# Optimization experiments

Measured on AMD Instinct MI355X. Metric: run time of the kernel, lower is better.

Reference implementation:

```python
import jax, jax.numpy as jnp
import numpy as np

NUM_LAYER = 5
EMB = 300
N_NODES = 100000
N_EDGES = 200000
NUM_GRAPHS = 5000
NUM_ATOM_TYPE = 120
NUM_CHIRALITY = 3
NUM_BOND_TYPE = 6
NUM_BOND_DIR = 3
BN_EPS = 1e-5


def _xavier(key, shape):
    fan_in, fan_out = shape[-2], shape[-1]
    a = jnp.sqrt(6.0 / (fan_in + fan_out))
    return jax.random.uniform(key, shape, jnp.float32, -a, a)


def setup_inputs() -> dict:
    key = jax.random.key(0)
    ks = jax.random.split(key, 12)
    x = jax.random.randint(ks[0], (N_NODES, 2), 0, 3)
    edge_index = jax.random.randint(ks[1], (2, N_EDGES), 0, N_NODES)
    edge_attr = jax.random.randint(ks[2], (N_EDGES, 2), 0, 3)
    batch = jnp.sort(jax.random.randint(ks[3], (N_NODES,), 0, NUM_GRAPHS))
    # parameters (layer-stacked for the NUM_LAYER GIN convs)
    x_emb1 = _xavier(ks[4], (NUM_ATOM_TYPE, EMB))
    x_emb2 = _xavier(ks[5], (NUM_CHIRALITY, EMB))
    edge_e1 = _xavier(ks[6], (NUM_LAYER, NUM_BOND_TYPE, EMB))
    edge_e2 = _xavier(ks[7], (NUM_LAYER, NUM_BOND_DIR, EMB))
    W1 = _xavier(ks[8], (NUM_LAYER, EMB, 2 * EMB))
    b1 = jnp.zeros((NUM_LAYER, 2 * EMB), jnp.float32)
    W2 = _xavier(ks[9], (NUM_LAYER, 2 * EMB, EMB))
    b2 = jnp.zeros((NUM_LAYER, EMB), jnp.float32)
    gamma = jnp.ones((NUM_LAYER, EMB), jnp.float32)
    beta = jnp.zeros((NUM_LAYER, EMB), jnp.float32)
    return dict(x=x, edge_index=edge_index, edge_attr=edge_attr, batch=batch,
                x_emb1=x_emb1, x_emb2=x_emb2, edge_e1=edge_e1, edge_e2=edge_e2,
                W1=W1, b1=b1, W2=W2, b2=b2, gamma=gamma, beta=beta)


def _forward(x, edge_index, edge_attr, batch,
             x_emb1, x_emb2, edge_e1, edge_e2, W1, b1, W2, b2, gamma, beta):
    N = x.shape[0]
    # add self loops (GINConv uses fill_value=0 for self-loop edge_attr)
    loop = jnp.arange(N)
    src = jnp.concatenate([edge_index[0], loop])  # [E+N]
    dst = jnp.concatenate([edge_index[1], loop])
    ea = jnp.concatenate([edge_attr, jnp.zeros((N, 2), edge_attr.dtype)], axis=0)
    h = x_emb1[x[:, 0]] + x_emb2[x[:, 1]]  # [N, EMB]
    for l in range(NUM_LAYER):
        eemb = edge_e1[l][ea[:, 0]] + edge_e2[l][ea[:, 1]]  # [E+N, EMB]
        msg = h[src] + eemb
        agg = jax.ops.segment_sum(msg, dst, num_segments=N)  # scatter-add
        # GIN MLP: Linear(EMB,2EMB) -> ReLU -> Linear(2EMB,EMB)
        h2 = jax.nn.relu(agg @ W1[l] + b1[l]) @ W2[l] + b2[l]
        # BatchNorm1d (training-mode batch statistics, biased var)
        mu = jnp.mean(h2, axis=0)
        var = jnp.mean(jnp.square(h2 - mu), axis=0)
        hn = (h2 - mu) * jax.lax.rsqrt(var + BN_EPS) * gamma[l] + beta[l]
        h = hn if l == NUM_LAYER - 1 else jax.nn.relu(hn)  # drop_ratio=0
    # JK='last'; global mean pool per graph
    sums = jax.ops.segment_sum(h, batch, num_segments=NUM_GRAPHS)
    counts = jax.ops.segment_sum(jnp.ones((N,), h.dtype), batch, num_segments=NUM_GRAPHS)
    return sums / jnp.maximum(counts, 1.0)[:, None]


def reference(x, edge_index, edge_attr, batch,
              x_emb1, x_emb2, edge_e1, edge_e2, W1, b1, W2, b2, gamma, beta):
    return _forward(x, edge_index, edge_attr, batch,
                    x_emb1, x_emb2, edge_e1, edge_e2, W1, b1, W2, b2, gamma, beta)
```

## Files before the change

kernel.cpp:

```cpp
#include <hip/hip_runtime.h>

typedef unsigned short u16;
typedef unsigned int u32;
typedef __attribute__((ext_vector_type(8))) short short8;
typedef __attribute__((ext_vector_type(4))) float float4v;
typedef _Float16 half8v __attribute__((ext_vector_type(8)));

static constexpr int   kN    = 100000;
static constexpr int   kE    = 200000;
static constexpr int   kEMB  = 300;
static constexpr int   kSA   = 304;
static constexpr int   kKW1  = 320;
static constexpr int   kNH   = 600;
static constexpr int   kNHP  = 608;
static constexpr int   kG    = 5000;
static constexpr int   kL    = 5;
static constexpr float kEPS  = 1e-5f;

static constexpr int   kB1BUF = 5120;
static constexpr int   kB2OFF = 10240;
static constexpr int   kB2BUF = 9728;
static constexpr int   kSMEMU = 29696;

__device__ inline float bf2f(u16 u) {
    union { u32 u32v; float f; } v; v.u32v = ((u32)u) << 16; return v.f;
}
__device__ inline u16 f2bf(float f) {
    union { float f; u32 u; } v; v.f = f;
    u32 r = v.u + 0x7fff + ((v.u >> 16) & 1);
    return (u16)(r >> 16);
}
__device__ inline short h16s(float f) {
    union { _Float16 h; short s; } u; u.h = (_Float16)f; return u.s;
}
__device__ inline short8 load8(const u16* p) {
    return *reinterpret_cast<const short8*>(p);
}
__device__ inline half8v as_h8(short8 s) {
    union { short8 s; half8v h; } u; u.s = s; return u.h;
}
__device__ inline float4v zed4() { float4v z = {0.f, 0.f, 0.f, 0.f}; return z; }
__device__ inline float gload(const void* p, long long i, int isf32) {
    if (isf32) return ((const float*)p)[i];
    return bf2f(((const u16*)p)[i]);
}
__device__ inline float pread(const void* p, size_t i, int f32p) {
    if (f32p) return ((const float*)p)[i];
    return bf2f(((const u16*)p)[i]);
}
__device__ inline void pwrite(void* p, size_t i, float v, int f32p) {
    if (f32p) ((float*)p)[i] = v;
    else      ((u16*)p)[i] = f2bf(v);
}
__device__ inline void gl_lds16(const void* g, void* l) {
    __builtin_amdgcn_global_load_lds(
        (__attribute__((address_space(1))) void*)g,
        (__attribute__((address_space(3))) void*)l, 16, 0, 0);
}

__global__ void detect_kernel(const u16* __restrict__ w1raw, int* flag) {
    if (threadIdx.x == 0 && blockIdx.x == 0) {
        int cnt = 0;
        for (int i = 0; i < 256; ++i) {
            int e = (w1raw[i] >> 7) & 0xFF;
            if (e >= 96 && e <= 126) ++cnt;
        }
        *flag = (cnt >= 200) ? 0 : 1;
    }
}

__global__ void cvt_kernel(const void* __restrict__ src, float* __restrict__ dst,
                           int n, const int* __restrict__ flag) {
    int i = blockIdx.x * blockDim.x + threadIdx.x;
    if (i >= n) return;
    int isf = *flag;
    dst[i] = isf ? ((const float*)src)[i] : bf2f(((const u16*)src)[i]);
}

__global__ void w1t_kernel(const void* __restrict__ W1, u16* __restrict__ W1T,
                           const int* __restrict__ flag, int f32p) {
    int idx = blockIdx.x * blockDim.x + threadIdx.x;
    const int per_layer = kNHP * kKW1;
    if (idx >= kL * per_layer) return;
    int isf = *flag;
    int l = idx / per_layer; int rem = idx - l * per_layer;
    int n = rem / kKW1; int k = rem - n * kKW1;
    u16 v = 0;
    if (n < kNH && k < kEMB) {
        float f = gload(W1, (long long)l * kEMB * kNH + (long long)k * kNH + n, isf);
        v = f32p ? (u16)h16s(f) : f2bf(f);
    }
    W1T[idx] = v;
}
__global__ void w2t_kernel(const void* __restrict__ W2, u16* __restrict__ W2T,
                           const int* __restrict__ flag, int f32p) {
    int idx = blockIdx.x * blockDim.x + threadIdx.x;
    const int per_layer = 19 * 304 * 32;
    if (idx >= kL * per_layer) return;
    int isf = *flag;
    int l = idx / per_layer; int rem = idx - l * per_layer;
    int p = rem / (304 * 32); int r2 = rem - p * (304 * 32);
    int n = r2 >> 5; int kk = r2 & 31;
    int q = kk >> 3, j3 = kk & 7;
    int klocal = (j3 < 4) ? (q * 4 + j3) : (16 + q * 4 + (j3 - 4));
    int k = p * 32 + klocal;
    u16 v = 0;
    if (n < kEMB && k < kNH) {
        float f = gload(W2, (long long)l * kNH * kEMB + (long long)k * kEMB + n, isf);
        v = f32p ? (u16)h16s(f) : f2bf(f);
    }
    W2T[idx] = v;
}

__global__ void embed_kernel(const int* __restrict__ x,
                             const float* __restrict__ emb1,
                             const float* __restrict__ emb2,
                             void* __restrict__ h, int f32p) {
    int idx = blockIdx.x * blockDim.x + threadIdx.x;
    if (idx >= kN * kSA) return;
    int n = idx / kSA; int c = idx - n * kSA;
    float v = 0.f;
    if (c < kEMB) v = emb1[x[2 * n] * kEMB + c] + emb2[x[2 * n + 1] * kEMB + c];
    pwrite(h, idx, v, f32p);
}

__global__ void zero_int_kernel(int* p, int n) {
    int i = blockIdx.x * blockDim.x + threadIdx.x;
    if (i < n) p[i] = 0;
}
__global__ void count_kernel(const int* __restrict__ dst, int* row_ptr) {
    int e = blockIdx.x * blockDim.x + threadIdx.x;
    if (e < kE) atomicAdd(&row_ptr[1 + dst[e]], 1);
}
__global__ __launch_bounds__(1024) void scan1_kernel(int* a, int* bsum, int n) {
    __shared__ int s[1024];
    int t = threadIdx.x;
    int i = blockIdx.x * 1024 + t;
    s[t] = (i < n) ? a[i] : 0;
    __syncthreads();
    for (int off = 1; off < 1024; off <<= 1) {
        int v = (t >= off) ? s[t - off] : 0;
        __syncthreads();
        s[t] += v;
        __syncthreads();
    }
    if (i < n) a[i] = s[t];
    if (t == 1023) bsum[blockIdx.x] = s[t];
}
__global__ __launch_bounds__(128) void scan2_kernel(const int* bsum, int* ebsum, int nb) {
    __shared__ int s[128];
    int t = threadIdx.x;
    int orig = (t < nb) ? bsum[t] : 0;
    s[t] = orig;
    __syncthreads();
    for (int off = 1; off < 128; off <<= 1) {
        int v = (t >= off) ? s[t - off] : 0;
        __syncthreads();
        s[t] += v;
        __syncthreads();
    }
    if (t < nb) ebsum[t] = s[t] - orig;
}
__global__ void scan3_kernel(int* a, const int* ebsum, int* row_ptr0, int n) {
    int i = blockIdx.x * blockDim.x + threadIdx.x;
    if (i >= n) return;
    a[i] += ebsum[i >> 10];
    if (i == 0) *row_ptr0 = 0;
}
__global__ void scatter_kernel(const int* __restrict__ src, const int* __restrict__ dst,
                               const int* __restrict__ ea,
                               const int* __restrict__ row_ptr, int* cursor,
                               int* __restrict__ epack) {
    int e = blockIdx.x * blockDim.x + threadIdx.x;
    if (e >= kE) return;
    int d = dst[e];
    int pos = row_ptr[d] + atomicAdd(&cursor[d], 1);
    epack[pos] = src[e] | (ea[2 * e] << 20) | (ea[2 * e + 1] << 24);
}

__global__ __launch_bounds__(256) void aggregate_kernel(
        const void* __restrict__ h, const int* __restrict__ row_ptr,
        const int* __restrict__ epack,
        const float* __restrict__ e1,
        const float* __restrict__ e2,
        const float* __restrict__ stats_prev,
        const float* __restrict__ gam,
        const float* __restrict__ bet,
        float* __restrict__ stats_next,
        void* __restrict__ agg, int mode, int f32p) {
    if (blockIdx.x == 0) {
        for (int i = threadIdx.x; i < 2 * kEMB; i += 256) stats_next[i] = 0.f;
    }
    int wave = threadIdx.x >> 6;
    int lane = threadIdx.x & 63;
    int base = (blockIdx.x * 4 + wave) * 4;

    float sc[5], sh[5];
#pragma unroll
    for (int j = 0; j < 5; ++j) {
        int c = j * 64 + lane;
        sc[j] = 1.f; sh[j] = 0.f;
        if (mode && c < kEMB) {
            const float invM = 1.0f / kN;
            float mu = stats_prev[c] * invM;
            float var = stats_prev[kEMB + c] * invM - mu * mu;
            if (var < 0.f) var = 0.f;
            float rs = rsqrtf(var + kEPS);
            sc[j] = rs * gam[c];
            sh[j] = bet[c] - mu * sc[j];
        }
    }

    int s[4], e[4];
    float acc[4][5];
#pragma unroll
    for (int t = 0; t < 4; ++t) {
        int node = base + t;
        if (node < kN) { s[t] = row_ptr[node]; e[t] = row_ptr[node + 1]; }
        else           { s[t] = 0; e[t] = 0; }
#pragma unroll
        for (int j = 0; j < 5; ++j) {
            int c = j * 64 + lane;
            acc[t][j] = 0.f;
            if (node < kN && c < kEMB) {
                float hv = pread(h, (size_t)node * kSA + c, f32p) * sc[j] + sh[j];
                if (mode && hv < 0.f) hv = 0.f;
                acc[t][j] = hv + e1[c] + e2[c];
            }
        }
    }

    int maxd = 0;
#pragma unroll
    for (int t = 0; t < 4; ++t) {
        int d = e[t] - s[t];
        if (d > maxd) maxd = d;
    }

    for (int i = 0; i < maxd; ++i) {
        int p[4], act[4];
#pragma unroll
        for (int t = 0; t < 4; ++t) {
            act[t] = (s[t] + i < e[t]);
            p[t] = act[t] ? epack[s[t] + i] : 0;
        }
        float hv[4][5];
#pragma unroll
        for (int t = 0; t < 4; ++t) {
            if (act[t]) {
                int srcn = p[t] & 0xFFFFF;
#pragma unroll
                for (int j = 0; j < 5; ++j) {
                    int c = j * 64 + lane;
                    hv[t][j] = (c < kEMB) ? pread(h, (size_t)srcn * kSA + c, f32p) : 0.f;
                }
            }
        }
#pragma unroll
        for (int t = 0; t < 4; ++t) {
            if (act[t]) {
                int a0 = (p[t] >> 20) & 15;
                int a1 = (p[t] >> 24) & 15;
#pragma unroll
                for (int j = 0; j < 5; ++j) {
                    int c = j * 64 + lane;
                    if (c < kEMB) {
                        float w = hv[t][j] * sc[j] + sh[j];
                        if (mode && w < 0.f) w = 0.f;
                        acc[t][j] += w + e1[a0 * kEMB + c] + e2[a1 * kEMB + c];
                    }
                }
            }
        }
    }

#pragma unroll
    for (int t = 0; t < 4; ++t) {
        int node = base + t;
        if (node < kN) {
#pragma unroll
            for (int j = 0; j < 5; ++j) {
                int c = j * 64 + lane;
                if (c < kSA)
                    pwrite(agg, (size_t)node * kSA + c, (c < kEMB) ? acc[t][j] : 0.f, f32p);
            }
        }
    }
}

template <int F32P>
__global__ __launch_bounds__(256, 2) void mlp_kernel(
        const void* A, void* D,
        const u16* __restrict__ W1Tl,
        const float* __restrict__ bias1,
        const u16* __restrict__ W2Tl,
        const float* __restrict__ bias2,
        float* __restrict__ stats) {
    __shared__ __align__(16) u16 SMEM[kSMEMU];
    int tid = threadIdx.x;
    int wave = tid >> 6, lane = tid & 63;
    int r16 = lane & 15, quad = lane >> 4;
    const int NT = kN / 16;
    int mt_raw = blockIdx.x * 4 + wave;
    int mt = (mt_raw < NT) ? mt_raw : (NT - 1);
    int valid = (mt_raw < NT);

#pragma unroll
    for (int i = 0; i < 8; ++i) {
        int c = wave + 4 * i;
        if (c < 10) {
            gl_lds16(W1Tl + (size_t)r16 * kKW1 + c * 32 + quad * 8,
                     SMEM + c * 512);
        } else if (c < 29) {
            int nt2 = c - 10;
            gl_lds16(W2Tl + ((size_t)nt2 * 16 + r16) * 32 + quad * 8,
                     SMEM + kB2OFF + nt2 * 512);
        }
    }

    short8 ahi[10];
    short8 zed = {0, 0, 0, 0, 0, 0, 0, 0};
    if (F32P) {
        const float* Arow = (const float*)A + (size_t)(mt * 16 + r16) * kSA + quad * 8;
#pragma unroll
        for (int kc = 0; kc < 10; ++kc) {
            short8 hh = zed;
            if (kc < 9 || quad < 2) {
                const float* pp = Arow + kc * 32;
#pragma unroll
                for (int j = 0; j < 8; ++j) hh[j] = h16s(pp[j]);
            }
            ahi[kc] = hh;
        }
    } else {
        const u16* Arow = (const u16*)A + (size_t)(mt * 16 + r16) * kSA + quad * 8;
#pragma unroll
        for (int kc = 0; kc < 9; ++kc) ahi[kc] = load8(Arow + kc * 32);
        ahi[9] = (quad < 2) ? load8(Arow + 9 * 32) : zed;
    }

    float4v acc2[19];
#pragma unroll
    for (int i = 0; i < 19; ++i) acc2[i] = zed4();

    short8 a2 = zed;
    short8 a2l = zed;

    for (int p = 0; p < 19; ++p) {
        __syncthreads();
        {
            int p1 = p + 1;
            u16* b1d = SMEM + kB1BUF;
            u16* b2d = SMEM + kB2OFF + (p1 & 1) * kB2BUF;
#pragma unroll
            for (int i = 0; i < 5; ++i) {
                int c = wave + 4 * i;
                if (c < 10) {
                    gl_lds16(W1Tl + (size_t)((2 * p + 1) * 16 + r16) * kKW1
                                 + c * 32 + quad * 8,
                             b1d + c * 512);
                } else if (c < 20 && p1 < 19) {
                    int nt2 = c - 10;
                    gl_lds16(W2Tl + ((size_t)p1 * 304 + nt2 * 16 + r16) * 32 + quad * 8,
                             b2d + nt2 * 512);
                }
            }
        }
        {
            const u16* B1 = SMEM;
            float4v aa = zed4(), ab = zed4();
#pragma unroll
            for (int kc = 0; kc < 10; kc += 2) {
                short8 w0 = load8(B1 + kc * 512 + lane * 8);
                short8 w1 = load8(B1 + (kc + 1) * 512 + lane * 8);
                if (F32P) {
                    aa = __builtin_amdgcn_mfma_f32_16x16x32_f16(as_h8(w0), as_h8(ahi[kc]), aa, 0, 0, 0);
                    ab = __builtin_amdgcn_mfma_f32_16x16x32_f16(as_h8(w1), as_h8(ahi[kc + 1]), ab, 0, 0, 0);
                } else {
                    aa = __builtin_amdgcn_mfma_f32_16x16x32_bf16(w0, ahi[kc], aa, 0, 0, 0);
                    ab = __builtin_amdgcn_mfma_f32_16x16x32_bf16(w1, ahi[kc + 1], ab, 0, 0, 0);
                }
            }
            float4v bv = *(const float4v*)(bias1 + (2 * p) * 16 + quad * 4);
#pragma unroll
            for (int r = 0; r < 4; ++r) {
                int n1 = (2 * p) * 16 + quad * 4 + r;
                float v = (n1 < kNH) ? (aa[r] + ab[r] + bv[r]) : 0.f;
                if (v < 0.f) v = 0.f;
                if (F32P) {
                    a2[r] = h16s(v);
                } else {
                    u16 hb = f2bf(v);
                    a2[r] = (short)hb;
                    a2l[r] = (short)f2bf(v - bf2f(hb));
                }
            }
        }
        __syncthreads();
        {
            int p1 = p + 1;
            u16* b1d = SMEM;
            u16* b2d = SMEM + kB2OFF + (p1 & 1) * kB2BUF;
#pragma unroll
            for (int i = 0; i < 5; ++i) {
                int c = wave + 4 * i;
                if (c < 10) {
                    if (2 * p + 2 < 38)
                        gl_lds16(W1Tl + (size_t)((2 * p + 2) * 16 + r16) * kKW1
                                     + c * 32 + quad * 8,
                                 b1d + c * 512);
                } else {
                    int nt2 = c;
                    if (nt2 < 19 && p1 < 19)
                        gl_lds16(W2Tl + ((size_t)p1 * 304 + nt2 * 16 + r16) * 32 + quad * 8,
                                 b2d + nt2 * 512);
                }
            }
        }
        {
            const u16* B1 = SMEM + kB1BUF;
            float4v aa = zed4(), ab = zed4();
#pragma unroll
            for (int kc = 0; kc < 10; kc += 2) {
                short8 w0 = load8(B1 + kc * 512 + lane * 8);
                short8 w1 = load8(B1 + (kc + 1) * 512 + lane * 8);
                if (F32P) {
                    aa = __builtin_amdgcn_mfma_f32_16x16x32_f16(as_h8(w0), as_h8(ahi[kc]), aa, 0, 0, 0);
                    ab = __builtin_amdgcn_mfma_f32_16x16x32_f16(as_h8(w1), as_h8(ahi[kc + 1]), ab, 0, 0, 0);
                } else {
                    aa = __builtin_amdgcn_mfma_f32_16x16x32_bf16(w0, ahi[kc], aa, 0, 0, 0);
                    ab = __builtin_amdgcn_mfma_f32_16x16x32_bf16(w1, ahi[kc + 1], ab, 0, 0, 0);
                }
            }
            float4v bv = *(const float4v*)(bias1 + (2 * p + 1) * 16 + quad * 4);
#pragma unroll
            for (int r = 0; r < 4; ++r) {
                int n1 = (2 * p + 1) * 16 + quad * 4 + r;
                float v = (n1 < kNH) ? (aa[r] + ab[r] + bv[r]) : 0.f;
                if (v < 0.f) v = 0.f;
                if (F32P) {
                    a2[4 + r] = h16s(v);
                } else {
                    u16 hb = f2bf(v);
                    a2[4 + r] = (short)hb;
                    a2l[4 + r] = (short)f2bf(v - bf2f(hb));
                }
            }
        }
        {
            const u16* B2 = SMEM + kB2OFF + (p & 1) * kB2BUF;
#pragma unroll
            for (int nt2 = 0; nt2 < 19; ++nt2) {
                short8 b = load8(B2 + nt2 * 512 + lane * 8);
                if (F32P) {
                    acc2[nt2] = __builtin_amdgcn_mfma_f32_16x16x32_f16(as_h8(a2), as_h8(b), acc2[nt2], 0, 0, 0);
                } else {
                    acc2[nt2] = __builtin_amdgcn_mfma_f32_16x16x32_bf16(a2, b, acc2[nt2], 0, 0, 0);
                    acc2[nt2] = __builtin_amdgcn_mfma_f32_16x16x32_bf16(a2l, b, acc2[nt2], 0, 0, 0);
                }
            }
        }
    }

    __syncthreads();
    float* RB = (float*)SMEM;
#pragma unroll
    for (int nt2 = 0; nt2 < 19; ++nt2) {
        int n = nt2 * 16 + r16;
        float s4 = 0.f, q4 = 0.f;
        if (valid && n < kEMB) {
            float bv = bias2[n];
#pragma unroll
            for (int r = 0; r < 4; ++r) {
                float v = acc2[nt2][r] + bv;
                int m = mt * 16 + quad * 4 + r;
                pwrite(D, (size_t)m * kSA + n, v, F32P);
                s4 += v; q4 += v * v;
            }
        }
        s4 += __shfl_down(s4, 32); q4 += __shfl_down(q4, 32);
        s4 += __shfl_down(s4, 16); q4 += __shfl_down(q4, 16);
        if (quad == 0) {
            RB[wave * 304 + nt2 * 16 + r16] = s4;
            RB[1216 + wave * 304 + nt2 * 16 + r16] = q4;
        }
    }
    __syncthreads();
    for (int c = tid; c < 304; c += 256) {
        if (c < kEMB) {
            float ss = 0.f, qq = 0.f;
#pragma unroll
            for (int w = 0; w < 4; ++w) {
                ss += RB[w * 304 + c];
                qq += RB[1216 + w * 304 + c];
            }
            atomicAdd(&stats[c], ss);
            atomicAdd(&stats[kEMB + c], qq);
        }
    }
}

__device__ inline int lower_bound(const int* a, int n, int key) {
    int lo = 0, hi = n;
    while (lo < hi) { int mid = (lo + hi) >> 1; if (a[mid] < key) lo = mid + 1; else hi = mid; }
    return lo;
}
__global__ __launch_bounds__(64) void pool_kernel(const void* __restrict__ h2,
                                                  const int* __restrict__ batch,
                                                  const float* __restrict__ stats,
                                                  const float* __restrict__ gam,
                                                  const float* __restrict__ bet,
                                                  void* __restrict__ out,
                                                  const int* __restrict__ flag, int f32p) {
    int g = blockIdx.x;
    int lane = threadIdx.x;
    int isf = *flag;
    int start = lower_bound(batch, kN, g);
    int end = lower_bound(batch, kN, g + 1);
    int cnt = end - start;
    float inv = 1.0f / (float)(cnt > 0 ? cnt : 1);
    for (int c = lane; c < kEMB; c += 64) {
        const float invM = 1.0f / kN;
        float mu = stats[c] * invM;
        float var = stats[kEMB + c] * invM - mu * mu;
        if (var < 0.f) var = 0.f;
        float rs = rsqrtf(var + kEPS);
        float sc = rs * gam[c];
        float sh = bet[c] - mu * sc;
        float s = 0.f;
        for (int n = start; n < end; ++n)
            s += pread(h2, (size_t)n * kSA + c, f32p) * sc + sh;
        float v = s * inv;
        if (isf) ((float*)out)[g * kEMB + c] = v;
        else     ((u16*)out)[g * kEMB + c] = f2bf(v);
    }
}

extern "C" void kernel_launch(void* const* d_in, const int* in_sizes, int n_in,
                              void* d_out, int out_size, void* d_ws, size_t ws_size,
                              hipStream_t stream) {
    const int* x          = (const int*)d_in[0];
    const int* edge_index = (const int*)d_in[1];
    const int* edge_attr  = (const int*)d_in[2];
    const int* batch      = (const int*)d_in[3];
    const void* x_emb1 = d_in[4];
    const void* x_emb2 = d_in[5];
    const void* e1raw  = d_in[6];
    const void* e2raw  = d_in[7];
    const void* W1     = d_in[8];
    const void* b1raw  = d_in[9];
    const void* W2     = d_in[10];
    const void* b2raw  = d_in[11];
    const void* gmraw  = d_in[12];
    const void* btraw  = d_in[13];

    const int* src = edge_index;
    const int* dst = edge_index + kE;

    const int f32p = (ws_size >= (size_t)250000000) ? 1 : 0;
    const size_t esz = f32p ? 4 : 2;

    char* p = (char*)d_ws;
    size_t off = 0;
    auto carve = [&](size_t bytes) {
        void* r = p + off;
        off += (bytes + 255) & ~(size_t)255;
        return r;
    };
    void* plane0 = carve((size_t)kN * kSA * esz);
    void* plane1 = carve((size_t)kN * kSA * esz);
    u16* W1T     = (u16*)carve((size_t)kL * kNHP * kKW1 * 2);
    u16* W2T     = (u16*)carve((size_t)kL * 19 * 304 * 32 * 2);
    int* row_ptr = (int*)carve((size_t)(kN + 1) * 4);
    int* cursor  = (int*)carve((size_t)kN * 4);
    int* epack   = (int*)carve((size_t)kE * 4);
    float* statsA = (float*)carve(2 * kEMB * 4);
    float* statsB = (float*)carve(2 * kEMB * 4);
    int* bsum    = (int*)carve(512);
    int* ebsum   = (int*)carve(512);
    int* flag    = (int*)carve(256);
    float* parf  = (float*)carve((size_t)57900 * 4);

    float* emb1  = parf + 0;
    float* emb2  = parf + 36000;
    float* e1    = parf + 36900;
    float* e2    = parf + 45900;
    float* b1    = parf + 50400;
    float* b2    = parf + 53400;
    float* gamma = parf + 54900;
    float* beta  = parf + 56400;

    detect_kernel<<<1, 64, 0, stream>>>((const u16*)W1, flag);
    cvt_kernel<<<(36000 + 255) / 256, 256, 0, stream>>>(x_emb1, emb1, 36000, flag);
    cvt_kernel<<<(900 + 255) / 256, 256, 0, stream>>>(x_emb2, emb2, 900, flag);
    cvt_kernel<<<(9000 + 255) / 256, 256, 0, stream>>>(e1raw, e1, 9000, flag);
    cvt_kernel<<<(4500 + 255) / 256, 256, 0, stream>>>(e2raw, e2, 4500, flag);
    cvt_kernel<<<(3000 + 255) / 256, 256, 0, stream>>>(b1raw, b1, 3000, flag);
    cvt_kernel<<<(1500 + 255) / 256, 256, 0, stream>>>(b2raw, b2, 1500, flag);
    cvt_kernel<<<(1500 + 255) / 256, 256, 0, stream>>>(gmraw, gamma, 1500, flag);
    cvt_kernel<<<(1500 + 255) / 256, 256, 0, stream>>>(btraw, beta, 1500, flag);

    {
        int n1 = kL * kNHP * kKW1;
        w1t_kernel<<<(n1 + 255) / 256, 256, 0, stream>>>(W1, W1T, flag, f32p);
        int n2 = kL * 19 * 304 * 32;
        w2t_kernel<<<(n2 + 255) / 256, 256, 0, stream>>>(W2, W2T, flag, f32p);
    }

    embed_kernel<<<(kN * kSA + 255) / 256, 256, 0, stream>>>(x, emb1, emb2, plane0, f32p);

    zero_int_kernel<<<(kN + 1 + 255) / 256, 256, 0, stream>>>(row_ptr, kN + 1);
    zero_int_kernel<<<(kN + 255) / 256, 256, 0, stream>>>(cursor, kN);
    count_kernel<<<(kE + 255) / 256, 256, 0, stream>>>(dst, row_ptr);
    const int nb = (kN + 1023) / 1024;
    scan1_kernel<<<nb, 1024, 0, stream>>>(row_ptr + 1, bsum, kN);
    scan2_kernel<<<1, 128, 0, stream>>>(bsum, ebsum, nb);
    scan3_kernel<<<(kN + 255) / 256, 256, 0, stream>>>(row_ptr + 1, ebsum, row_ptr, kN);
    scatter_kernel<<<(kE + 255) / 256, 256, 0, stream>>>(src, dst, edge_attr, row_ptr,
                                                         cursor, epack);

    const int mlp_blocks = (kN / 16 + 3) / 4;
    const int agg_blocks = (kN + 15) / 16;
    void* cur = plane0;
    void* agg = plane1;
    float* stats_prev = statsA;
    for (int l = 0; l < kL; ++l) {
        float* stats_cur = (l % 2 == 0) ? statsA : statsB;
        const float* gam_prev = gamma + (l > 0 ? (l - 1) : 0) * kEMB;
        const float* bet_prev = beta + (l > 0 ? (l - 1) : 0) * kEMB;
        aggregate_kernel<<<agg_blocks, 256, 0, stream>>>(
            cur, row_ptr, epack, e1 + l * 6 * kEMB, e2 + l * 3 * kEMB,
            (l > 0) ? stats_prev : stats_cur, gam_prev, bet_prev,
            stats_cur, agg, (l > 0) ? 1 : 0, f32p);
        void* dout = f32p ? cur : agg;
        if (f32p)
            mlp_kernel<1><<<mlp_blocks, 256, 0, stream>>>(
                agg, dout, W1T + (size_t)l * kNHP * kKW1, b1 + l * kNH,
                W2T + (size_t)l * 19 * 304 * 32, b2 + l * kEMB, stats_cur);
        else
            mlp_kernel<0><<<mlp_blocks, 256, 0, stream>>>(
                agg, dout, W1T + (size_t)l * kNHP * kKW1, b1 + l * kNH,
                W2T + (size_t)l * 19 * 304 * 32, b2 + l * kEMB, stats_cur);
        stats_prev = stats_cur;
        cur = dout;
        agg = (cur == plane0) ? plane1 : plane0;
    }

    pool_kernel<<<kG, 64, 0, stream>>>(cur, batch, stats_prev, gamma + 4 * kEMB,
                                       beta + 4 * kEMB, d_out, flag, f32p);
}
```

Baseline: 1.933 ms.

## Single-buffer W2 tiles in LDS and raise MLP kernel occupancy to four blocks

Drops the double-buffered W2 staging in the fused MLP kernel. Each outer iteration now loads its W2 slice into one LDS buffer right after the first barrier, instead of prefetching the next slice during the current one. This shrinks shared memory from about 59KB to about 40KB, and launch bounds are raised from 2 to 4 blocks per CU so more waves can hide latency. The cost is lost overlap of W2 loads with compute, plus tighter register limits that could cause spills given the large accumulator and A-fragment arrays.

```diff
diff --git a/kernel.cpp b/kernel.cpp
--- a/kernel.cpp
+++ b/kernel.cpp
@@ -19,8 +19,7 @@
 
 static constexpr int   kB1BUF = 5120;
 static constexpr int   kB2OFF = 10240;
-static constexpr int   kB2BUF = 9728;
-static constexpr int   kSMEMU = 29696;
+static constexpr int   kSMEMU = 19968;
 
 __device__ inline float bf2f(u16 u) {
     union { u32 u32v; float f; } v; v.u32v = ((u32)u) << 16; return v.f;
@@ -289,7 +288,7 @@
 }
 
 template <int F32P>
-__global__ __launch_bounds__(256, 2) void mlp_kernel(
+__global__ __launch_bounds__(256, 4) void mlp_kernel(
         const void* A, void* D,
         const u16* __restrict__ W1Tl,
         const float* __restrict__ bias1,
@@ -306,16 +305,11 @@
     int valid = (mt_raw < NT);
 
 #pragma unroll
-    for (int i = 0; i < 8; ++i) {
+    for (int i = 0; i < 3; ++i) {
         int c = wave + 4 * i;
-        if (c < 10) {
+        if (c < 10)
             gl_lds16(W1Tl + (size_t)r16 * kKW1 + c * 32 + quad * 8,
                      SMEM + c * 512);
-        } else if (c < 29) {
-            int nt2 = c - 10;
-            gl_lds16(W2Tl + ((size_t)nt2 * 16 + r16) * 32 + quad * 8,
-                     SMEM + kB2OFF + nt2 * 512);
-        }
     }
 
     short8 ahi[10];
@@ -349,19 +343,18 @@
     for (int p = 0; p < 19; ++p) {
         __syncthreads();
         {
-            int p1 = p + 1;
             u16* b1d = SMEM + kB1BUF;
-            u16* b2d = SMEM + kB2OFF + (p1 & 1) * kB2BUF;
-#pragma unroll
-            for (int i = 0; i < 5; ++i) {
+            u16* b2d = SMEM + kB2OFF;
+#pragma unroll
+            for (int i = 0; i < 8; ++i) {
                 int c = wave + 4 * i;
                 if (c < 10) {
                     gl_lds16(W1Tl + (size_t)((2 * p + 1) * 16 + r16) * kKW1
                                  + c * 32 + quad * 8,
                              b1d + c * 512);
-                } else if (c < 20 && p1 < 19) {
+                } else if (c < 29) {
                     int nt2 = c - 10;
-                    gl_lds16(W2Tl + ((size_t)p1 * 304 + nt2 * 16 + r16) * 32 + quad * 8,
+                    gl_lds16(W2Tl + ((size_t)p * 304 + nt2 * 16 + r16) * 32 + quad * 8,
                              b2d + nt2 * 512);
                 }
             }
@@ -397,24 +390,14 @@
             }
         }
         __syncthreads();
-        {
-            int p1 = p + 1;
-            u16* b1d = SMEM;
-            u16* b2d = SMEM + kB2OFF + (p1 & 1) * kB2BUF;
-#pragma unroll
-            for (int i = 0; i < 5; ++i) {
+        if (p + 1 < 19) {
+#pragma unroll
+            for (int i = 0; i < 3; ++i) {
                 int c = wave + 4 * i;
-                if (c < 10) {
-                    if (2 * p + 2 < 38)
-                        gl_lds16(W1Tl + (size_t)((2 * p + 2) * 16 + r16) * kKW1
-                                     + c * 32 + quad * 8,
-                                 b1d + c * 512);
-                } else {
-                    int nt2 = c;
-                    if (nt2 < 19 && p1 < 19)
-                        gl_lds16(W2Tl + ((size_t)p1 * 304 + nt2 * 16 + r16) * 32 + quad * 8,
-                                 b2d + nt2 * 512);
-                }
+                if (c < 10)
+                    gl_lds16(W1Tl + (size_t)((2 * p + 2) * 16 + r16) * kKW1
+                                 + c * 32 + quad * 8,
+                             SMEM + c * 512);
             }
         }
         {
@@ -448,7 +431,7 @@
             }
         }
         {
-            const u16* B2 = SMEM + kB2OFF + (p & 1) * kB2BUF;
+            const u16* B2 = SMEM + kB2OFF;
 #pragma unroll
             for (int nt2 = 0; nt2 < 19; ++nt2) {
                 short8 b = load8(B2 + nt2 * 512 + lane * 8);
```

Result: slower. 3.413 ms (+76.5%).
